# Kernel tuning notes

Measured on AMD Instinct MI355X. Metric: run time of the kernel, lower is better.

The kernel has to match this reference:

```python
import jax, jax.numpy as jnp
import numpy as np

B, CIN, IMG = 8, 512, 112
P = IMG // 14          # patch_size = 8
NP = 14 * 14           # n_patch = 196
DEC, SKIP, EMB = 512, 512, 768
BN_EPS = 1e-3          # keras BatchNormalization default
IN_EPS = 1e-3          # tfa InstanceNormalization default


def conv2d(x, w, b, stride=1):
    # x: NCHW, w: OIHW
    y = jax.lax.conv_general_dilated(x, w, (stride, stride), 'VALID',
                                     dimension_numbers=('NCHW', 'OIHW', 'NCHW'))
    return y + b[None, :, None, None]


def bn_inf(x, g, b, m, v):
    scale = g / jnp.sqrt(v + BN_EPS)
    return (x - m[None, :, None, None]) * scale[None, :, None, None] + b[None, :, None, None]


def setup_inputs() -> dict:
    key = jax.random.key(0)
    ks = jax.random.split(key, 20)
    s = 0.05
    return {
        'decoder': jax.random.normal(ks[0], (B, CIN, IMG, IMG), jnp.float32),
        'trans': jax.random.normal(ks[1], (B, NP, EMB), jnp.float32),
        'pe_w': jax.random.normal(ks[2], (DEC, CIN, P, P), jnp.float32) * s,
        'pe_b': jax.random.normal(ks[3], (DEC,), jnp.float32) * s,
        'mc_w': jax.random.normal(ks[4], (SKIP, CIN, 1, 1), jnp.float32) * s,
        'mc_b': jax.random.normal(ks[5], (SKIP,), jnp.float32) * s,
        'bn1_g': jax.random.uniform(ks[6], (SKIP,), jnp.float32, 0.5, 1.5),
        'bn1_b': jax.random.normal(ks[7], (SKIP,), jnp.float32) * s,
        'bn1_m': jax.random.normal(ks[8], (SKIP,), jnp.float32) * s,
        'bn1_v': jax.random.uniform(ks[9], (SKIP,), jnp.float32, 0.5, 1.5),
        'wq': jax.random.normal(ks[10], (DEC, SKIP), jnp.float32) * s,
        'wk': jax.random.normal(ks[11], (EMB, SKIP), jnp.float32) * s,
        'wv': jax.random.normal(ks[12], (EMB, SKIP), jnp.float32) * s,
        'wo': jax.random.normal(ks[13], (SKIP, SKIP), jnp.float32) * s,
        'psi_g': jnp.ones((1,), jnp.float32),
        'psi_b': jnp.zeros((1,), jnp.float32),
        'rc_w': jax.random.normal(ks[14], (SKIP, SKIP, 1, 1), jnp.float32) * s,
        'rc_b': jax.random.normal(ks[15], (SKIP,), jnp.float32) * s,
        'bn2_g': jax.random.uniform(ks[16], (SKIP,), jnp.float32, 0.5, 1.5),
        'bn2_b': jax.random.normal(ks[17], (SKIP,), jnp.float32) * s,
        'bn2_m': jax.random.normal(ks[18], (SKIP,), jnp.float32) * s,
        'bn2_v': jax.random.uniform(ks[19], (SKIP,), jnp.float32, 0.5, 1.5),
    }


def reference(decoder, trans, pe_w, pe_b, mc_w, mc_b, bn1_g, bn1_b, bn1_m, bn1_v,
              wq, wk, wv, wo, psi_g, psi_b, rc_w, rc_b, bn2_g, bn2_b, bn2_m, bn2_v):
    # mask branch: 1x1 conv + BN + ReLU  -> [B, SKIP, IMG, IMG]
    mask = jax.nn.relu(bn_inf(conv2d(decoder, mc_w, mc_b), bn1_g, bn1_b, bn1_m, bn1_v))

    # patch embedding: strided conv -> [B, DEC, 14, 14] -> tokens [B, NP, DEC]
    dl = conv2d(decoder, pe_w, pe_b, stride=P)
    dl = dl.reshape(dl.shape[0], dl.shape[1], -1).transpose(0, 2, 1)

    q = jnp.einsum('bnd,ds->bsn', dl, wq)       # [B, SKIP, NP]
    k = jnp.einsum('bne,es->bns', trans, wk)    # [B, NP, SKIP]
    v = jnp.einsum('bne,es->bsn', trans, wv)    # [B, SKIP, NP]

    sim = jnp.einsum('bsn,bnt->bst', q, k)      # [B, SKIP, SKIP]
    # InstanceNorm over the (SKIP, SKIP) map per sample (single channel)
    mu = sim.mean(axis=(1, 2), keepdims=True)
    var = sim.var(axis=(1, 2), keepdims=True)
    sim = (sim - mu) / jnp.sqrt(var + IN_EPS) * psi_g[0] + psi_b[0]
    sim = jax.nn.softmax(sim, axis=-1)

    out = jnp.einsum('bst,btn->bns', sim, v)    # [B, NP, SKIP]
    out = jnp.einsum('bns,so->bno', out, wo)    # [B, NP, SKIP]

    # reconstruct: tokens -> [B, SKIP, 14, 14] -> nearest upsample x P -> 1x1 conv + BN + ReLU
    x = out.transpose(0, 2, 1).reshape(out.shape[0], SKIP, 14, 14)
    x = jnp.repeat(jnp.repeat(x, P, axis=2), P, axis=3)
    x = jax.nn.relu(bn_inf(conv2d(x, rc_w, rc_b), bn2_g, bn2_b, bn2_m, bn2_v))

    return x * mask
```

## Files before the change

### kernel.cpp

```cpp
#include <hip/hip_runtime.h>
#include <stdint.h>

typedef __attribute__((ext_vector_type(8))) short v8s;
typedef __attribute__((ext_vector_type(4))) float v4f;

__device__ __forceinline__ uint16_t f2bf(float x){
  uint32_t u = __float_as_uint(x);
  return (uint16_t)((u + 0x7FFFu + ((u >> 16) & 1u)) >> 16);
}
__device__ __forceinline__ uint32_t pk2(float a, float b){
  return (uint32_t)f2bf(a) | ((uint32_t)f2bf(b) << 16);
}
__device__ __forceinline__ int swz(int e){ return e ^ (((e >> 7) & 3) << 3); }

__device__ __forceinline__ void gl16(const uint16_t* g, uint16_t* l){
  __builtin_amdgcn_global_load_lds((const __attribute__((address_space(1))) void*)g,
                                   (__attribute__((address_space(3))) void*)l, 16, 0, 0);
}

__global__ void __launch_bounds__(256) dra_cvt(const float* __restrict__ s,
                                               uint16_t* __restrict__ d, int n8){
  int i = blockIdx.x * 256 + threadIdx.x;
  if (i >= n8) return;
  const float4* sp = (const float4*)(s + (size_t)i * 8);
  float4 f0 = sp[0], f1 = sp[1];
  uint4 u; u.x = pk2(f0.x, f0.y); u.y = pk2(f0.z, f0.w);
  u.z = pk2(f1.x, f1.y); u.w = pk2(f1.z, f1.w);
  *(uint4*)(d + (size_t)i * 8) = u;
}

__global__ void __launch_bounds__(256) dra_tcvt(const float* __restrict__ s,
                                                uint16_t* __restrict__ d, int R, int C){
  int r8 = R >> 3;
  int id = blockIdx.x * 256 + threadIdx.x;
  if (id >= C * r8) return;
  int c = id / r8, r0 = (id - c * r8) * 8;
  float v[8];
  #pragma unroll
  for (int e = 0; e < 8; e++) v[e] = s[(size_t)(r0 + e) * C + c];
  uint4 u; u.x = pk2(v[0], v[1]); u.y = pk2(v[2], v[3]);
  u.z = pk2(v[4], v[5]); u.w = pk2(v[6], v[7]);
  *(uint4*)(d + (size_t)c * R + r0) = u;
}

__global__ void __launch_bounds__(256) dra_tdec(const float* __restrict__ dec,
                                                uint16_t* __restrict__ decT){
  __shared__ uint16_t lt[64 * 80];
  int t = threadIdx.x;
  int pos0 = blockIdx.x * 64;
  int ci0  = blockIdx.y * 64;
  int b    = blockIdx.z;
  #pragma unroll
  for (int i = 0; i < 4; i++){
    int idx = t + i * 256;
    int ci_l = idx >> 4, p4 = (idx & 15) * 4;
    const float4 f = *(const float4*)(dec + ((size_t)(b * 512 + ci0 + ci_l)) * 12544 + pos0 + p4);
    lt[(p4 + 0) * 80 + ci_l] = f2bf(f.x);
    lt[(p4 + 1) * 80 + ci_l] = f2bf(f.y);
    lt[(p4 + 2) * 80 + ci_l] = f2bf(f.z);
    lt[(p4 + 3) * 80 + ci_l] = f2bf(f.w);
  }
  __syncthreads();
  #pragma unroll
  for (int i = 0; i < 2; i++){
    int idx = t + i * 256;
    int p_l = idx >> 3, u = idx & 7;
    uint4 v = *(const uint4*)&lt[p_l * 80 + u * 8];
    *(uint4*)(decT + ((size_t)b * 12544 + pos0 + p_l) * 512 + ci0 + u * 8) = v;
  }
}

__global__ void __launch_bounds__(256) dra_wpe2(const float* __restrict__ pw,
                                                uint16_t* __restrict__ w2){
  int id = blockIdx.x * 256 + threadIdx.x;
  if (id >= 2097152) return;
  int co = id >> 12, rem = id & 4095;
  int ci8 = rem >> 6, pix = rem & 63;
  const float* s = pw + (size_t)co * 32768 + ci8 * 512 + pix;
  float v[8];
  #pragma unroll
  for (int j = 0; j < 8; j++) v[j] = s[j * 64];
  uint4 u; u.x = pk2(v[0], v[1]); u.y = pk2(v[2], v[3]);
  u.z = pk2(v[4], v[5]); u.w = pk2(v[6], v[7]);
  *(uint4*)(w2 + (size_t)co * 32768 + pix * 512 + ci8 * 8) = u;
}

__global__ void __launch_bounds__(256) dra_transb(const float* __restrict__ tr,
                                                  uint16_t* __restrict__ d){
  int id = blockIdx.x * 256 + threadIdx.x;
  if (id >= 1792 * 96) return;
  int n = id / 96, e0 = (id - n * 96) * 8;
  int b = n / 224, nl = n - b * 224;
  uint4 u = {0u,0u,0u,0u};
  if (nl < 196){
    const float* sp = tr + ((size_t)(b * 196 + nl)) * 768 + e0;
    u.x = pk2(sp[0], sp[1]); u.y = pk2(sp[2], sp[3]);
    u.z = pk2(sp[4], sp[5]); u.w = pk2(sp[6], sp[7]);
  }
  *(uint4*)(d + (size_t)n * 768 + e0) = u;
}

__global__ void dra_scales(const float* mcb, const float* g1, const float* b1,
                           const float* m1, const float* v1,
                           const float* rcb, const float* g2, const float* b2,
                           const float* m2, const float* v2,
                           float* s1, float* o1, float* s2, float* o2){
  int i = blockIdx.x * 256 + threadIdx.x;
  if (i >= 512) return;
  float sc1 = g1[i] / sqrtf(v1[i] + 1e-3f);
  s1[i] = sc1; o1[i] = (mcb[i] - m1[i]) * sc1 + b1[i];
  float sc2 = g2[i] / sqrtf(v2[i] + 1e-3f);
  s2[i] = sc2; o2[i] = (rcb[i] - m2[i]) * sc2 + b2[i];
}

__global__ void __launch_bounds__(256, 4) dra_k1(const uint16_t* __restrict__ decT,
    const uint16_t* __restrict__ wpe2, float* __restrict__ part)
{
  __shared__ uint16_t lA[2][128 * 32];
  __shared__ uint16_t lB[2][128 * 32];
  int t = threadIdx.x;
  int L = blockIdx.x;
  int x = L & 7, n = L >> 3;
  int shi = n / 56, rem = n - shi * 56;
  int tok_t = rem >> 2, co_t = rem & 3;
  int s    = shi * 8 + x;
  int bco  = co_t * 128;
  int tok0 = tok_t * 128;
  int lane = t & 63, w = t >> 6;
  int wm = w >> 1, wn = w & 1;
  int lr = lane & 15, lg = lane >> 4;

  const uint16_t* aB[2]; const uint16_t* bB[2]; int uu[2];
  #pragma unroll
  for (int i = 0; i < 2; i++){
    int u = t + i * 256; uu[i] = u;
    int row = u >> 2, h = u & 3;
    int token = tok0 + row;
    int b = token / 224, tl = token - b * 224;
    if (tl > 195) tl = 195;
    int py = tl / 14, px = tl - py * 14;
    aB[i] = decT + ((size_t)b * 12544 + py * 896 + px * 8) * 512 + h * 8;
    bB[i] = wpe2 + (size_t)(bco + row) * 32768 + s * 2048 + h * 8;
  }

  const v4f vzero = {0.f,0.f,0.f,0.f};
  v4f acc[4][4];
  #pragma unroll
  for (int i = 0; i < 4; i++)
    #pragma unroll
    for (int j = 0; j < 4; j++) acc[i][j] = vzero;

  auto stage = [&](int kk, int pb){
    int pix = s * 4 + (kk >> 4);
    int pa = ((pix >> 3) * 112 + (pix & 7)) * 512 + ((kk & 15) << 5);
    int pbo = kk << 5;
    gl16(aB[0] + pa,  &lA[pb][uu[0] * 8]);
    gl16(aB[1] + pa,  &lA[pb][uu[1] * 8]);
    gl16(bB[0] + pbo, &lB[pb][uu[0] * 8]);
    gl16(bB[1] + pbo, &lB[pb][uu[1] * 8]);
  };

  stage(0, 0);
  __syncthreads();
  int cur = 0;
  for (int kk = 0; kk < 64; ++kk){
    if (kk + 1 < 64) stage(kk + 1, cur ^ 1);
    v8s av[4], bv[4];
    #pragma unroll
    for (int mf = 0; mf < 4; mf++) av[mf] = *(const v8s*)&lA[cur][(wm*64 + mf*16 + lr) * 32 + lg * 8];
    #pragma unroll
    for (int nf = 0; nf < 4; nf++) bv[nf] = *(const v8s*)&lB[cur][(wn*64 + nf*16 + lr) * 32 + lg * 8];
    #pragma unroll
    for (int mf = 0; mf < 4; mf++)
      #pragma unroll
      for (int nf = 0; nf < 4; nf++)
        acc[mf][nf] = __builtin_amdgcn_mfma_f32_16x16x32_bf16(av[mf], bv[nf], acc[mf][nf], 0, 0, 0);
    __syncthreads();
    cur ^= 1;
  }

  float* pd = part + (size_t)s * 917504;
  #pragma unroll
  for (int mf = 0; mf < 4; mf++){
    #pragma unroll
    for (int nf = 0; nf < 4; nf++){
      int tokg = tok0 + wm*64 + mf*16 + lg*4;
      int cog  = bco  + wn*64 + nf*16 + lr;
      #pragma unroll
      for (int r = 0; r < 4; r++)
        pd[(size_t)(tokg + r) * 512 + cog] = acc[mf][nf][r];
    }
  }
}

__global__ void __launch_bounds__(256) dra_red(const float* __restrict__ part,
    const float* __restrict__ peb, uint16_t* __restrict__ dlb){
  int id = blockIdx.x * 256 + threadIdx.x;
  if (id >= 114688) return;
  int tok = id >> 6, c8 = (id & 63) * 8;
  float a0=0,a1=0,a2=0,a3=0,a4=0,a5=0,a6=0,a7=0;
  #pragma unroll
  for (int s = 0; s < 16; s++){
    const float* p = part + (size_t)s * 917504 + (size_t)tok * 512 + c8;
    float4 x = *(const float4*)p, y = *(const float4*)(p + 4);
    a0 += x.x; a1 += x.y; a2 += x.z; a3 += x.w;
    a4 += y.x; a5 += y.y; a6 += y.z; a7 += y.w;
  }
  const float4 b0 = *(const float4*)(peb + c8), b1 = *(const float4*)(peb + c8 + 4);
  uint4 o; o.x = pk2(a0 + b0.x, a1 + b0.y); o.y = pk2(a2 + b0.z, a3 + b0.w);
  o.z = pk2(a4 + b1.x, a5 + b1.y); o.w = pk2(a6 + b1.z, a7 + b1.w);
  *(uint4*)(dlb + (size_t)tok * 512 + c8) = o;
}

template<int MREP>
__global__ void __launch_bounds__(256, 2) dra_gemm(
    const uint16_t* __restrict__ A, const uint16_t* __restrict__ Bn, void* __restrict__ Dv,
    int M, int N, int K, int lda, int ldb, int ldd,
    long long sAz, long long sBz, long long sDz,
    int epi, const float* __restrict__ svec, const float* __restrict__ ovec)
{
  constexpr int BM = MREP * 32;
  __shared__ uint16_t lA[BM * 32];
  __shared__ uint16_t lB[64 * 32];
  int t = threadIdx.x, z = blockIdx.z;
  int bm = blockIdx.x * BM, bn = blockIdx.y * 64;
  const uint16_t* Az = A + (size_t)z * sAz;
  const uint16_t* Bz = Bn + (size_t)z * sBz;
  int lane = t & 63, w = t >> 6;
  int wm = w >> 1, wn = w & 1;
  int lr = lane & 15, lg = lane >> 4;
  const v4f vzero = {0.f, 0.f, 0.f, 0.f};
  v4f acc[MREP][2];
  #pragma unroll
  for (int i = 0; i < MREP; i++){ acc[i][0] = vzero; acc[i][1] = vzero; }

  for (int k0 = 0; k0 < K; k0 += 32){
    #pragma unroll
    for (int i = 0; i < MREP/2; i++){
      int idx = t + i * 256;
      int r = idx >> 2, ko = (idx & 3) << 3;
      int rg = bm + r; if (rg >= M) rg = M - 1;
      *(uint4*)&lA[swz(r * 32 + ko)] = *(const uint4*)(Az + (size_t)rg * lda + k0 + ko);
    }
    {
      int r = t >> 2, ko = (t & 3) << 3;
      *(uint4*)&lB[swz(r * 32 + ko)] = *(const uint4*)(Bz + (size_t)(bn + r) * ldb + k0 + ko);
    }
    __syncthreads();
    v8s av[MREP], bv[2];
    #pragma unroll
    for (int mf = 0; mf < MREP; mf++)
      av[mf] = *(const v8s*)&lA[swz((wm*(MREP*16) + mf*16 + lr) * 32 + lg * 8)];
    #pragma unroll
    for (int nf = 0; nf < 2; nf++)
      bv[nf] = *(const v8s*)&lB[swz((wn*32 + nf*16 + lr) * 32 + lg * 8)];
    #pragma unroll
    for (int mf = 0; mf < MREP; mf++)
      #pragma unroll
      for (int nf = 0; nf < 2; nf++)
        acc[mf][nf] = __builtin_amdgcn_mfma_f32_16x16x32_bf16(av[mf], bv[nf], acc[mf][nf], 0, 0, 0);
    __syncthreads();
  }

  #pragma unroll
  for (int mf = 0; mf < MREP; mf++){
    #pragma unroll
    for (int nf = 0; nf < 2; nf++){
      int mg0 = bm + wm*(MREP*16) + mf*16 + lg*4;
      int ng  = bn + wn*32 + nf*16 + lr;
      #pragma unroll
      for (int r = 0; r < 4; r++){
        int mg = mg0 + r;
        if (mg < M){
          float val = acc[mf][nf][r];
          size_t di = (size_t)z * sDz + (size_t)mg * ldd + ng;
          if (epi == 0)      ((float*)Dv)[di] = val;
          else if (epi == 1) ((uint16_t*)Dv)[di] = f2bf(val);
          else ((float*)Dv)[di] = fmaxf(val * svec[mg] + ovec[mg], 0.f);
        }
      }
    }
  }
}

__global__ void __launch_bounds__(256) dra_stats1(const float* __restrict__ sim,
                                                  double* __restrict__ ps){
  __shared__ double d1[256], d2[256];
  int b = blockIdx.y, blk = blockIdx.x, t = threadIdx.x;
  const float* s = sim + (size_t)b * 262144 + (size_t)blk * 2048 + t * 8;
  float4 x = *(const float4*)s, y = *(const float4*)(s + 4);
  double p1 = (double)x.x + x.y + x.z + x.w + y.x + y.y + y.z + y.w;
  double p2 = (double)x.x*x.x + (double)x.y*x.y + (double)x.z*x.z + (double)x.w*x.w
            + (double)y.x*y.x + (double)y.y*y.y + (double)y.z*y.z + (double)y.w*y.w;
  d1[t] = p1; d2[t] = p2;
  __syncthreads();
  for (int o = 128; o > 0; o >>= 1){
    if (t < o){ d1[t] += d1[t + o]; d2[t] += d2[t + o]; }
    __syncthreads();
  }
  if (t == 0){
    ps[(b * 128 + blk) * 2 + 0] = d1[0];
    ps[(b * 128 + blk) * 2 + 1] = d2[0];
  }
}

__global__ void __launch_bounds__(128) dra_stats2(const double* __restrict__ ps,
    const float* __restrict__ psig, const float* __restrict__ psib, float* __restrict__ ac){
  __shared__ double d1[128], d2[128];
  int b = blockIdx.x, t = threadIdx.x;
  d1[t] = ps[(b * 128 + t) * 2 + 0];
  d2[t] = ps[(b * 128 + t) * 2 + 1];
  __syncthreads();
  for (int o = 64; o > 0; o >>= 1){
    if (t < o){ d1[t] += d1[t + o]; d2[t] += d2[t + o]; }
    __syncthreads();
  }
  if (t == 0){
    double mean = d1[0] * (1.0 / 262144.0);
    double var  = d2[0] * (1.0 / 262144.0) - mean * mean;
    float a = psig[0] / (float)sqrt(var + 1e-3);
    ac[b * 2 + 0] = a;
    ac[b * 2 + 1] = psib[0] - (float)mean * a;
  }
}

__global__ void __launch_bounds__(256) dra_soft(const float* __restrict__ sim,
    const float* __restrict__ ac, uint16_t* __restrict__ P){
  int srow = blockIdx.x, b = blockIdx.y, t = threadIdx.x;
  const float* row = sim + (size_t)b * 262144 + (size_t)srow * 512;
  float a = ac[b * 2], c = ac[b * 2 + 1];
  float v0 = row[t] * a + c, v1 = row[t + 256] * a + c;
  __shared__ float red[256];
  red[t] = fmaxf(v0, v1);
  __syncthreads();
  for (int o = 128; o > 0; o >>= 1){
    if (t < o) red[t] = fmaxf(red[t], red[t + o]);
    __syncthreads();
  }
  float m = red[0];
  __syncthreads();
  float e0 = __expf(v0 - m), e1 = __expf(v1 - m);
  red[t] = e0 + e1;
  __syncthreads();
  for (int o = 128; o > 0; o >>= 1){
    if (t < o) red[t] += red[t + o];
    __syncthreads();
  }
  float inv = 1.f / red[0];
  uint16_t* pr = P + (size_t)b * 262144 + (size_t)srow * 512;
  pr[t] = f2bf(e0 * inv); pr[t + 256] = f2bf(e1 * inv);
}

__global__ void __launch_bounds__(256, 4) dra_k3(const uint16_t* __restrict__ decT,
    const uint16_t* __restrict__ mcw, const float* __restrict__ s1,
    const float* __restrict__ o1, const float* __restrict__ recon,
    float* __restrict__ outp)
{
  __shared__ uint16_t lA[2][128 * 32];
  __shared__ uint16_t lB[2][128 * 32];
  int t = threadIdx.x;
  int L = blockIdx.x;
  int x = L & 7, n = L >> 3;
  int co_t = n & 3, pg = n >> 2;
  int p = pg * 8 + x;
  int bz = p / 98, pt = p - bz * 98;
  int bco  = co_t * 128;
  int pos0 = pt * 128;
  int lane = t & 63, w = t >> 6;
  int wm = w >> 1, wn = w & 1;
  int lr = lane & 15, lg = lane >> 4;

  const uint16_t* aB[2]; const uint16_t* bB[2]; int uu[2];
  #pragma unroll
  for (int i = 0; i < 2; i++){
    int u = t + i * 256; uu[i] = u;
    int row = u >> 2, h = u & 3;
    aB[i] = mcw  + (size_t)(bco + row) * 512 + h * 8;
    bB[i] = decT + ((size_t)bz * 12544 + pos0 + row) * 512 + h * 8;
  }

  const v4f vzero = {0.f,0.f,0.f,0.f};
  v4f acc[4][4];
  #pragma unroll
  for (int i = 0; i < 4; i++)
    #pragma unroll
    for (int j = 0; j < 4; j++) acc[i][j] = vzero;

  auto stage = [&](int kk, int pb){
    int ko = kk << 5;
    gl16(aB[0] + ko, &lA[pb][uu[0] * 8]);
    gl16(aB[1] + ko, &lA[pb][uu[1] * 8]);
    gl16(bB[0] + ko, &lB[pb][uu[0] * 8]);
    gl16(bB[1] + ko, &lB[pb][uu[1] * 8]);
  };

  stage(0, 0);
  __syncthreads();
  int cur = 0;
  for (int kk = 0; kk < 16; ++kk){
    if (kk + 1 < 16) stage(kk + 1, cur ^ 1);
    v8s av[4], bv[4];
    #pragma unroll
    for (int mf = 0; mf < 4; mf++) av[mf] = *(const v8s*)&lA[cur][(wm*64 + mf*16 + lr) * 32 + lg * 8];
    #pragma unroll
    for (int nf = 0; nf < 4; nf++) bv[nf] = *(const v8s*)&lB[cur][(wn*64 + nf*16 + lr) * 32 + lg * 8];
    #pragma unroll
    for (int mf = 0; mf < 4; mf++)
      #pragma unroll
      for (int nf = 0; nf < 4; nf++)
        acc[mf][nf] = __builtin_amdgcn_mfma_f32_16x16x32_bf16(av[mf], bv[nf], acc[mf][nf], 0, 0, 0);
    __syncthreads();
    cur ^= 1;
  }

  #pragma unroll
  for (int mf = 0; mf < 4; mf++){
    #pragma unroll
    for (int r = 0; r < 4; r++){
      int co = bco + wm*64 + mf*16 + lg*4 + r;
      float sc = s1[co], of = o1[co];
      const float* rrow = recon + (size_t)co * 1792 + bz * 224;
      #pragma unroll
      for (int nf = 0; nf < 4; nf++){
        int pos = pos0 + wn*64 + nf*16 + lr;
        int h = pos / 112, wd = pos - h * 112;
        int pcol = (h >> 3) * 14 + (wd >> 3);
        float mask = fmaxf(acc[mf][nf][r] * sc + of, 0.f);
        outp[((size_t)(bz * 512 + co)) * 12544 + pos] = mask * rrow[pcol];
      }
    }
  }
}

extern "C" void kernel_launch(void* const* d_in, const int* in_sizes, int n_in,
                              void* d_out, int out_size, void* d_ws, size_t ws_size,
                              hipStream_t stream) {
  (void)in_sizes; (void)n_in; (void)out_size; (void)ws_size;
  const float* dec   = (const float*)d_in[0];
  const float* trans = (const float*)d_in[1];
  const float* pe_w  = (const float*)d_in[2];
  const float* pe_b  = (const float*)d_in[3];
  const float* mc_w  = (const float*)d_in[4];
  const float* mc_b  = (const float*)d_in[5];
  const float* bn1g  = (const float*)d_in[6];
  const float* bn1b  = (const float*)d_in[7];
  const float* bn1m  = (const float*)d_in[8];
  const float* bn1v  = (const float*)d_in[9];
  const float* wq    = (const float*)d_in[10];
  const float* wk    = (const float*)d_in[11];
  const float* wv    = (const float*)d_in[12];
  const float* wo    = (const float*)d_in[13];
  const float* psig  = (const float*)d_in[14];
  const float* psib  = (const float*)d_in[15];
  const float* rc_w  = (const float*)d_in[16];
  const float* rc_b  = (const float*)d_in[17];
  const float* bn2g  = (const float*)d_in[18];
  const float* bn2b  = (const float*)d_in[19];
  const float* bn2m  = (const float*)d_in[20];
  const float* bn2v  = (const float*)d_in[21];

  char* p = (char*)d_ws;
  auto take = [&](size_t bytes) -> void* {
    void* r = (void*)p; p += (bytes + 255) & ~(size_t)255; return r;
  };
  uint16_t* decT   = (uint16_t*)take((size_t)8 * 12544 * 512 * 2);
  uint16_t* wpe2   = (uint16_t*)take((size_t)512 * 32768 * 2);
  uint16_t* mcw    = (uint16_t*)take((size_t)512 * 512 * 2);
  uint16_t* rcw    = (uint16_t*)take((size_t)512 * 512 * 2);
  uint16_t* wqT    = (uint16_t*)take((size_t)512 * 512 * 2);
  uint16_t* woT    = (uint16_t*)take((size_t)512 * 512 * 2);
  uint16_t* wkT    = (uint16_t*)take((size_t)512 * 768 * 2);
  uint16_t* wvT    = (uint16_t*)take((size_t)512 * 768 * 2);
  uint16_t* transb = (uint16_t*)take((size_t)1792 * 768 * 2);
  float*    s1v    = (float*)take(512 * 4);
  float*    o1v    = (float*)take(512 * 4);
  float*    s2v    = (float*)take(512 * 4);
  float*    o2v    = (float*)take(512 * 4);
  uint16_t* dlb    = (uint16_t*)take((size_t)1792 * 512 * 2);
  uint16_t* Qt     = (uint16_t*)take((size_t)512 * 1792 * 2);
  uint16_t* Kt     = (uint16_t*)take((size_t)512 * 1792 * 2);
  uint16_t* Vb     = (uint16_t*)take((size_t)1792 * 512 * 2);
  float*    ac     = (float*)take(256);
  double*   ps     = (double*)take((size_t)8 * 128 * 2 * 8);
  float*    part   = (float*)take((size_t)16 * 1792 * 512 * 4);
  float*    simb   = part;
  uint16_t* P      = (uint16_t*)(part + 2097152);
  uint16_t* outb   = P + 2097152;
  uint16_t* out2   = outb + 917504;
  float*    recon  = (float*)(out2 + 917504);

  dra_tdec<<<dim3(196, 8, 8), 256, 0, stream>>>(dec, decT);
  dra_wpe2<<<8192, 256, 0, stream>>>(pe_w, wpe2);
  dra_cvt<<<128, 256, 0, stream>>>(mc_w, mcw, 32768);
  dra_cvt<<<128, 256, 0, stream>>>(rc_w, rcw, 32768);
  dra_tcvt<<<128, 256, 0, stream>>>(wq, wqT, 512, 512);
  dra_tcvt<<<192, 256, 0, stream>>>(wk, wkT, 768, 512);
  dra_tcvt<<<192, 256, 0, stream>>>(wv, wvT, 768, 512);
  dra_tcvt<<<128, 256, 0, stream>>>(wo, woT, 512, 512);
  dra_transb<<<672, 256, 0, stream>>>(trans, transb);
  dra_scales<<<2, 256, 0, stream>>>(mc_b, bn1g, bn1b, bn1m, bn1v,
                                    rc_b, bn2g, bn2b, bn2m, bn2v, s1v, o1v, s2v, o2v);

  dra_k1<<<896, 256, 0, stream>>>(decT, wpe2, part);
  dra_red<<<448, 256, 0, stream>>>(part, pe_b, dlb);

  dra_gemm<2><<<dim3(8, 28, 1), 256, 0, stream>>>(wqT, dlb, Qt, 512, 1792, 512,
      512, 512, 1792, 0, 0, 0, 1, nullptr, nullptr);
  dra_gemm<2><<<dim3(8, 28, 1), 256, 0, stream>>>(wkT, transb, Kt, 512, 1792, 768,
      768, 768, 1792, 0, 0, 0, 1, nullptr, nullptr);
  dra_gemm<2><<<dim3(28, 8, 1), 256, 0, stream>>>(transb, wvT, Vb, 1792, 512, 768,
      768, 768, 512, 0, 0, 0, 1, nullptr, nullptr);

  dra_gemm<2><<<dim3(8, 8, 8), 256, 0, stream>>>(Qt, Kt, simb, 512, 512, 224,
      1792, 1792, 512, 224, 224, 262144, 0, nullptr, nullptr);
  dra_stats1<<<dim3(128, 8), 256, 0, stream>>>(simb, ps);
  dra_stats2<<<8, 128, 0, stream>>>(ps, psig, psib, ac);
  dra_soft<<<dim3(512, 8), 256, 0, stream>>>(simb, ac, P);

  dra_gemm<2><<<dim3(4, 8, 8), 256, 0, stream>>>(Vb, P, outb, 224, 512, 512,
      512, 512, 512, 114688, 262144, 114688, 1, nullptr, nullptr);
  dra_gemm<2><<<dim3(28, 8, 1), 256, 0, stream>>>(outb, woT, out2, 1792, 512, 512,
      512, 512, 512, 0, 0, 0, 1, nullptr, nullptr);
  dra_gemm<2><<<dim3(8, 28, 1), 256, 0, stream>>>(rcw, out2, recon, 512, 1792, 512,
      512, 512, 1792, 0, 0, 0, 2, s2v, o2v);

  dra_k3<<<3136, 256, 0, stream>>>(decT, mcw, s1v, o1v, recon, (float*)d_out);
}
```

Before: 442.3 us.

## Triple-buffer LDS with swizzled layout and fine-grained waitcnt in GEMM kernels

Both MFMA GEMM kernels (patch-embed and 1x1 mask conv) move from double to triple buffered LDS staging. Each iteration now prefetches two stages ahead and waits with explicit vmcnt counts instead of a full __syncthreads. The LDS layout is XOR-swizzled on the 8-element chunk index to cut bank conflicts on the MFMA operand reads. The goal is more overlap of global-to-LDS loads with compute, at the cost of more LDS per block and a lower occupancy bound (3 instead of 4).

```diff
diff --git a/kernel.cpp b/kernel.cpp
--- a/kernel.cpp
+++ b/kernel.cpp
@@ -113,11 +113,11 @@
   s2[i] = sc2; o2[i] = (rcb[i] - m2[i]) * sc2 + b2[i];
 }
 
-__global__ void __launch_bounds__(256, 4) dra_k1(const uint16_t* __restrict__ decT,
+__global__ void __launch_bounds__(256, 3) dra_k1(const uint16_t* __restrict__ decT,
     const uint16_t* __restrict__ wpe2, float* __restrict__ part)
 {
-  __shared__ uint16_t lA[2][128 * 32];
-  __shared__ uint16_t lB[2][128 * 32];
+  __shared__ uint16_t lA[3][128 * 32];
+  __shared__ uint16_t lB[3][128 * 32];
   int t = threadIdx.x;
   int L = blockIdx.x;
   int x = L & 7, n = L >> 3;
@@ -135,12 +135,13 @@
   for (int i = 0; i < 2; i++){
     int u = t + i * 256; uu[i] = u;
     int row = u >> 2, h = u & 3;
+    int hs = h ^ ((row >> 1) & 3);
     int token = tok0 + row;
     int b = token / 224, tl = token - b * 224;
     if (tl > 195) tl = 195;
     int py = tl / 14, px = tl - py * 14;
-    aB[i] = decT + ((size_t)b * 12544 + py * 896 + px * 8) * 512 + h * 8;
-    bB[i] = wpe2 + (size_t)(bco + row) * 32768 + s * 2048 + h * 8;
+    aB[i] = decT + ((size_t)b * 12544 + py * 896 + px * 8) * 512 + hs * 8;
+    bB[i] = wpe2 + (size_t)(bco + row) * 32768 + s * 2048 + hs * 8;
   }
 
   const v4f vzero = {0.f,0.f,0.f,0.f};
@@ -160,23 +161,44 @@
     gl16(bB[1] + pbo, &lB[pb][uu[1] * 8]);
   };
 
-  stage(0, 0);
-  __syncthreads();
-  int cur = 0;
+  int aoff[4], boff[4];
+  #pragma unroll
+  for (int mf = 0; mf < 4; mf++){
+    int R = wm*64 + mf*16 + lr;
+    aoff[mf] = R * 32 + (lg ^ ((R >> 1) & 3)) * 8;
+  }
+  #pragma unroll
+  for (int nf = 0; nf < 4; nf++){
+    int R = wn*64 + nf*16 + lr;
+    boff[nf] = R * 32 + (lg ^ ((R >> 1) & 3)) * 8;
+  }
+
+  stage(0, 0); stage(1, 1);
+  asm volatile("s_waitcnt vmcnt(4)" ::: "memory");
+  __builtin_amdgcn_s_barrier();
+  __builtin_amdgcn_sched_barrier(0);
+
+  int cur = 0, nxt = 2;
   for (int kk = 0; kk < 64; ++kk){
-    if (kk + 1 < 64) stage(kk + 1, cur ^ 1);
     v8s av[4], bv[4];
     #pragma unroll
-    for (int mf = 0; mf < 4; mf++) av[mf] = *(const v8s*)&lA[cur][(wm*64 + mf*16 + lr) * 32 + lg * 8];
-    #pragma unroll
-    for (int nf = 0; nf < 4; nf++) bv[nf] = *(const v8s*)&lB[cur][(wn*64 + nf*16 + lr) * 32 + lg * 8];
+    for (int mf = 0; mf < 4; mf++) av[mf] = *(const v8s*)&lA[cur][aoff[mf]];
+    #pragma unroll
+    for (int nf = 0; nf < 4; nf++) bv[nf] = *(const v8s*)&lB[cur][boff[nf]];
     #pragma unroll
     for (int mf = 0; mf < 4; mf++)
       #pragma unroll
       for (int nf = 0; nf < 4; nf++)
         acc[mf][nf] = __builtin_amdgcn_mfma_f32_16x16x32_bf16(av[mf], bv[nf], acc[mf][nf], 0, 0, 0);
-    __syncthreads();
-    cur ^= 1;
+    if (kk + 2 < 64) stage(kk + 2, nxt);
+    if (kk < 63){
+      if (kk < 62) asm volatile("s_waitcnt vmcnt(4) lgkmcnt(0)" ::: "memory");
+      else         asm volatile("s_waitcnt vmcnt(0) lgkmcnt(0)" ::: "memory");
+      __builtin_amdgcn_s_barrier();
+      __builtin_amdgcn_sched_barrier(0);
+    }
+    cur = (cur == 2) ? 0 : cur + 1;
+    nxt = (nxt == 2) ? 0 : nxt + 1;
   }
 
   float* pd = part + (size_t)s * 917504;
@@ -351,13 +373,13 @@
   pr[t] = f2bf(e0 * inv); pr[t + 256] = f2bf(e1 * inv);
 }
 
-__global__ void __launch_bounds__(256, 4) dra_k3(const uint16_t* __restrict__ decT,
+__global__ void __launch_bounds__(256, 3) dra_k3(const uint16_t* __restrict__ decT,
     const uint16_t* __restrict__ mcw, const float* __restrict__ s1,
     const float* __restrict__ o1, const float* __restrict__ recon,
     float* __restrict__ outp)
 {
-  __shared__ uint16_t lA[2][128 * 32];
-  __shared__ uint16_t lB[2][128 * 32];
+  __shared__ uint16_t lA[3][128 * 32];
+  __shared__ uint16_t lB[3][128 * 32];
   int t = threadIdx.x;
   int L = blockIdx.x;
   int x = L & 7, n = L >> 3;
@@ -375,8 +397,9 @@
   for (int i = 0; i < 2; i++){
     int u = t + i * 256; uu[i] = u;
     int row = u >> 2, h = u & 3;
-    aB[i] = mcw  + (size_t)(bco + row) * 512 + h * 8;
-    bB[i] = decT + ((size_t)bz * 12544 + pos0 + row) * 512 + h * 8;
+    int hs = h ^ ((row >> 1) & 3);
+    aB[i] = mcw  + (size_t)(bco + row) * 512 + hs * 8;
+    bB[i] = decT + ((size_t)bz * 12544 + pos0 + row) * 512 + hs * 8;
   }
 
   const v4f vzero = {0.f,0.f,0.f,0.f};
@@ -394,23 +417,44 @@
     gl16(bB[1] + ko, &lB[pb][uu[1] * 8]);
   };
 
-  stage(0, 0);
-  __syncthreads();
-  int cur = 0;
+  int aoff[4], boff[4];
+  #pragma unroll
+  for (int mf = 0; mf < 4; mf++){
+    int R = wm*64 + mf*16 + lr;
+    aoff[mf] = R * 32 + (lg ^ ((R >> 1) & 3)) * 8;
+  }
+  #pragma unroll
+  for (int nf = 0; nf < 4; nf++){
+    int R = wn*64 + nf*16 + lr;
+    boff[nf] = R * 32 + (lg ^ ((R >> 1) & 3)) * 8;
+  }
+
+  stage(0, 0); stage(1, 1);
+  asm volatile("s_waitcnt vmcnt(4)" ::: "memory");
+  __builtin_amdgcn_s_barrier();
+  __builtin_amdgcn_sched_barrier(0);
+
+  int cur = 0, nxt = 2;
   for (int kk = 0; kk < 16; ++kk){
-    if (kk + 1 < 16) stage(kk + 1, cur ^ 1);
     v8s av[4], bv[4];
     #pragma unroll
-    for (int mf = 0; mf < 4; mf++) av[mf] = *(const v8s*)&lA[cur][(wm*64 + mf*16 + lr) * 32 + lg * 8];
-    #pragma unroll
-    for (int nf = 0; nf < 4; nf++) bv[nf] = *(const v8s*)&lB[cur][(wn*64 + nf*16 + lr) * 32 + lg * 8];
+    for (int mf = 0; mf < 4; mf++) av[mf] = *(const v8s*)&lA[cur][aoff[mf]];
+    #pragma unroll
+    for (int nf = 0; nf < 4; nf++) bv[nf] = *(const v8s*)&lB[cur][boff[nf]];
     #pragma unroll
     for (int mf = 0; mf < 4; mf++)
       #pragma unroll
       for (int nf = 0; nf < 4; nf++)
         acc[mf][nf] = __builtin_amdgcn_mfma_f32_16x16x32_bf16(av[mf], bv[nf], acc[mf][nf], 0, 0, 0);
-    __syncthreads();
-    cur ^= 1;
+    if (kk + 2 < 16) stage(kk + 2, nxt);
+    if (kk < 15){
+      if (kk < 14) asm volatile("s_waitcnt vmcnt(4) lgkmcnt(0)" ::: "memory");
+      else         asm volatile("s_waitcnt vmcnt(0) lgkmcnt(0)" ::: "memory");
+      __builtin_amdgcn_s_barrier();
+      __builtin_amdgcn_sched_barrier(0);
+    }
+    cur = (cur == 2) ? 0 : cur + 1;
+    nxt = (nxt == 2) ? 0 : nxt + 1;
   }
 
   #pragma unroll
```

After: 437.3 us. About the same (-1.1%).

## Load weight operands directly from global and swizzle LDS activation tiles

Applied to the files above, without the earlier changes.

In the patch-embed GEMM and the 1x1 mask-conv GEMM, the weight operand is now read straight from global memory into registers instead of being staged through LDS, which halves LDS usage and global-to-LDS traffic per block. The remaining LDS-staged activation tile gets an XOR swizzle on its 16-byte chunks to reduce bank conflicts on the MFMA fragment reads. The cost is that weight reads now come from global or L2 per wave, with no double buffering to hide their latency, and each wave re-reads weights that used to be shared across the block.

```diff
diff --git a/kernel.cpp b/kernel.cpp
--- a/kernel.cpp
+++ b/kernel.cpp
@@ -117,7 +117,6 @@
     const uint16_t* __restrict__ wpe2, float* __restrict__ part)
 {
   __shared__ uint16_t lA[2][128 * 32];
-  __shared__ uint16_t lB[2][128 * 32];
   int t = threadIdx.x;
   int L = blockIdx.x;
   int x = L & 7, n = L >> 3;
@@ -130,18 +129,22 @@
   int wm = w >> 1, wn = w & 1;
   int lr = lane & 15, lg = lane >> 4;
 
-  const uint16_t* aB[2]; const uint16_t* bB[2]; int uu[2];
+  const uint16_t* aB[2]; int uu[2];
   #pragma unroll
   for (int i = 0; i < 2; i++){
     int u = t + i * 256; uu[i] = u;
     int row = u >> 2, h = u & 3;
+    int hs = h ^ ((row >> 1) & 3);
     int token = tok0 + row;
     int b = token / 224, tl = token - b * 224;
     if (tl > 195) tl = 195;
     int py = tl / 14, px = tl - py * 14;
-    aB[i] = decT + ((size_t)b * 12544 + py * 896 + px * 8) * 512 + h * 8;
-    bB[i] = wpe2 + (size_t)(bco + row) * 32768 + s * 2048 + h * 8;
-  }
+    aB[i] = decT + ((size_t)b * 12544 + py * 896 + px * 8) * 512 + hs * 8;
+  }
+  const uint16_t* bP[4];
+  #pragma unroll
+  for (int nf = 0; nf < 4; nf++)
+    bP[nf] = wpe2 + (size_t)(bco + wn*64 + nf*16 + lr) * 32768 + s * 2048 + lg * 8;
 
   const v4f vzero = {0.f,0.f,0.f,0.f};
   v4f acc[4][4];
@@ -153,12 +156,16 @@
   auto stage = [&](int kk, int pb){
     int pix = s * 4 + (kk >> 4);
     int pa = ((pix >> 3) * 112 + (pix & 7)) * 512 + ((kk & 15) << 5);
-    int pbo = kk << 5;
-    gl16(aB[0] + pa,  &lA[pb][uu[0] * 8]);
-    gl16(aB[1] + pa,  &lA[pb][uu[1] * 8]);
-    gl16(bB[0] + pbo, &lB[pb][uu[0] * 8]);
-    gl16(bB[1] + pbo, &lB[pb][uu[1] * 8]);
+    gl16(aB[0] + pa, &lA[pb][uu[0] * 8]);
+    gl16(aB[1] + pa, &lA[pb][uu[1] * 8]);
   };
+
+  int aoff[4];
+  #pragma unroll
+  for (int mf = 0; mf < 4; mf++){
+    int R = wm*64 + mf*16 + lr;
+    aoff[mf] = R * 32 + (lg ^ ((R >> 1) & 3)) * 8;
+  }
 
   stage(0, 0);
   __syncthreads();
@@ -167,9 +174,9 @@
     if (kk + 1 < 64) stage(kk + 1, cur ^ 1);
     v8s av[4], bv[4];
     #pragma unroll
-    for (int mf = 0; mf < 4; mf++) av[mf] = *(const v8s*)&lA[cur][(wm*64 + mf*16 + lr) * 32 + lg * 8];
-    #pragma unroll
-    for (int nf = 0; nf < 4; nf++) bv[nf] = *(const v8s*)&lB[cur][(wn*64 + nf*16 + lr) * 32 + lg * 8];
+    for (int mf = 0; mf < 4; mf++) av[mf] = *(const v8s*)&lA[cur][aoff[mf]];
+    #pragma unroll
+    for (int nf = 0; nf < 4; nf++) bv[nf] = *(const v8s*)(bP[nf] + (kk << 5));
     #pragma unroll
     for (int mf = 0; mf < 4; mf++)
       #pragma unroll
@@ -356,7 +363,6 @@
     const float* __restrict__ o1, const float* __restrict__ recon,
     float* __restrict__ outp)
 {
-  __shared__ uint16_t lA[2][128 * 32];
   __shared__ uint16_t lB[2][128 * 32];
   int t = threadIdx.x;
   int L = blockIdx.x;
@@ -370,14 +376,18 @@
   int wm = w >> 1, wn = w & 1;
   int lr = lane & 15, lg = lane >> 4;
 
-  const uint16_t* aB[2]; const uint16_t* bB[2]; int uu[2];
+  const uint16_t* bB[2]; int uu[2];
   #pragma unroll
   for (int i = 0; i < 2; i++){
     int u = t + i * 256; uu[i] = u;
     int row = u >> 2, h = u & 3;
-    aB[i] = mcw  + (size_t)(bco + row) * 512 + h * 8;
-    bB[i] = decT + ((size_t)bz * 12544 + pos0 + row) * 512 + h * 8;
-  }
+    int hs = h ^ ((row >> 1) & 3);
+    bB[i] = decT + ((size_t)bz * 12544 + pos0 + row) * 512 + hs * 8;
+  }
+  const uint16_t* aP[4];
+  #pragma unroll
+  for (int mf = 0; mf < 4; mf++)
+    aP[mf] = mcw + (size_t)(bco + wm*64 + mf*16 + lr) * 512 + lg * 8;
 
   const v4f vzero = {0.f,0.f,0.f,0.f};
   v4f acc[4][4];
@@ -388,11 +398,16 @@
 
   auto stage = [&](int kk, int pb){
     int ko = kk << 5;
-    gl16(aB[0] + ko, &lA[pb][uu[0] * 8]);
-    gl16(aB[1] + ko, &lA[pb][uu[1] * 8]);
     gl16(bB[0] + ko, &lB[pb][uu[0] * 8]);
     gl16(bB[1] + ko, &lB[pb][uu[1] * 8]);
   };
+
+  int boff[4];
+  #pragma unroll
+  for (int nf = 0; nf < 4; nf++){
+    int R = wn*64 + nf*16 + lr;
+    boff[nf] = R * 32 + (lg ^ ((R >> 1) & 3)) * 8;
+  }
 
   stage(0, 0);
   __syncthreads();
@@ -401,9 +416,9 @@
     if (kk + 1 < 16) stage(kk + 1, cur ^ 1);
     v8s av[4], bv[4];
     #pragma unroll
-    for (int mf = 0; mf < 4; mf++) av[mf] = *(const v8s*)&lA[cur][(wm*64 + mf*16 + lr) * 32 + lg * 8];
-    #pragma unroll
-    for (int nf = 0; nf < 4; nf++) bv[nf] = *(const v8s*)&lB[cur][(wn*64 + nf*16 + lr) * 32 + lg * 8];
+    for (int mf = 0; mf < 4; mf++) av[mf] = *(const v8s*)(aP[mf] + (kk << 5));
+    #pragma unroll
+    for (int nf = 0; nf < 4; nf++) bv[nf] = *(const v8s*)&lB[cur][boff[nf]];
     #pragma unroll
     for (int mf = 0; mf < 4; mf++)
       #pragma unroll
```

New measurement: 543.4 us. 1.23x slower.
